# Kernel tuning notes

Measured on AMD Instinct MI355X. Metric: run time of the kernel, lower is better.

Reference implementation:

```python
import jax, jax.numpy as jnp
import numpy as np

N = 12288      # num nodes == in_num_dim (num_center_nodes)
D_IN = 512     # in_node_dim
D_EMB = 128    # embed_dim
D_OUT = 64     # out_dim
E = 393216     # num edges (avg degree 32)
NEG_SLOPE = 0.2  # GATConv default negative_slope


def _glorot(k, shape):
    lim = float(np.sqrt(6.0 / (shape[0] + shape[1])))
    return jax.random.uniform(k, shape, jnp.float32, -lim, lim)


def setup_inputs() -> dict:
    key = jax.random.key(0)
    ks = jax.random.split(key, 13)
    x = jax.random.normal(ks[0], (N, D_IN), jnp.float32)
    edge_index = jax.random.randint(ks[1], (2, E), 0, N, jnp.int64)
    # StructureAE.dense: Linear(in_node_dim, embed_dim)
    W_s1 = _glorot(ks[2], (D_EMB, D_IN))
    b_s1 = jnp.zeros((D_EMB,), jnp.float32)
    # GATConv(embed_dim, out_dim): heads=1, concat, bias
    W_g = _glorot(ks[3], (D_OUT, D_EMB))
    a_src = _glorot(ks[4], (D_OUT, 1))[:, 0]
    a_dst = _glorot(ks[5], (D_OUT, 1))[:, 0]
    b_g = jnp.zeros((D_OUT,), jnp.float32)
    # AttributeAE: dense1 = Linear(N, embed_dim), dense2 = Linear(embed_dim, out_dim)
    W_a1 = _glorot(ks[6], (D_EMB, N))
    b_a1 = jnp.zeros((D_EMB,), jnp.float32)
    W_a2 = _glorot(ks[7], (D_OUT, D_EMB))
    b_a2 = jnp.zeros((D_OUT,), jnp.float32)
    return dict(x=x, W_s1=W_s1, b_s1=b_s1, W_g=W_g, a_src=a_src, a_dst=a_dst,
                b_g=b_g, W_a1=W_a1, b_a1=b_a1, W_a2=W_a2, b_a2=b_a2,
                edge_index=edge_index, batch_size=N)


def _gat(x1, W_g, a_src, a_dst, b_g, edge_index):
    """Single-head GATConv with self-loops (PyG defaults)."""
    n = x1.shape[0]
    g = x1 @ W_g.T                                   # [N, D_OUT]
    loops = jnp.arange(n, dtype=edge_index.dtype)
    src = jnp.concatenate([edge_index[0], loops])    # message source j
    dst = jnp.concatenate([edge_index[1], loops])    # message target i
    sc_src = g @ a_src                               # [N]
    sc_dst = g @ a_dst                               # [N]
    e = jax.nn.leaky_relu(sc_src[src] + sc_dst[dst], NEG_SLOPE)  # [E+N]
    m = jax.ops.segment_max(e, dst, num_segments=n)
    e = jnp.exp(e - m[dst])
    denom = jax.ops.segment_sum(e, dst, num_segments=n)
    alpha = e / denom[dst]                           # softmax per target node
    h = jax.ops.segment_sum(alpha[:, None] * g[src], dst, num_segments=n)
    return h + b_g


def reference(x, W_s1, b_s1, W_g, a_src, a_dst, b_g,
              W_a1, b_a1, W_a2, b_a2, edge_index, batch_size):
    n = x.shape[0]
    # StructureAE (dropout=0 -> identity)
    x1 = jax.nn.relu(x @ W_s1.T + b_s1)              # [N, D_EMB]
    h = _gat(x1, W_g, a_src, a_dst, b_g, edge_index)  # [N, D_OUT]
    s_ = jax.nn.sigmoid(h @ h.T)                     # [N, N]
    # AttributeAE on x[:num_center_nodes] (pad if batch smaller)
    xp = x if batch_size >= n else jnp.pad(x, ((0, n - batch_size), (0, 0)))
    xt = jax.nn.relu(xp.T @ W_a1.T + b_a1)           # [D_IN, D_EMB]
    xa = xt @ W_a2.T + b_a2                          # [D_IN, D_OUT]
    x_ = h @ xa.T                                    # [N, D_IN]
    return (x_, s_)
```

## Files before the change

kernel.cpp:

```cpp
#include <hip/hip_runtime.h>
#include <cstddef>
#include <cstdint>

#define N_NODES 12288
#define D_IN    512
#define D_EMB   128
#define D_OUT   64
#define NEDGE   393216

typedef __attribute__((ext_vector_type(8))) short short8;
typedef __attribute__((ext_vector_type(4))) float f32x4;

__device__ __forceinline__ ushort f2bf(float f) {
  uint32_t u = __float_as_uint(f);
  u += 0x7fffu + ((u >> 16) & 1u);
  return (ushort)(u >> 16);
}
__device__ __forceinline__ float bf2f(ushort h) {
  return __uint_as_float((uint32_t)h << 16);
}

__device__ __forceinline__ void conv4(const float* __restrict__ src,
    ushort* __restrict__ hi, ushort* __restrict__ lo, int idx)
{
  float4 v = *(const float4*)(src + idx);
  const float* pv = &v.x;
  ushort4 h, l;
  ushort* ph = &h.x; ushort* pl = &l.x;
#pragma unroll
  for (int q = 0; q < 4; ++q) {
    ph[q] = f2bf(pv[q]);
    pl[q] = f2bf(pv[q] - bf2f(ph[q]));
  }
  *(ushort4*)(hi + idx) = h;
  *(ushort4*)(lo + idx) = l;
}

template<int MODE>
__device__ __forceinline__ void mfma_tile64(
    int lane, int i0, int j0,
    const ushort* __restrict__ Ahi, const ushort* __restrict__ Alo,
    const ushort* __restrict__ Bhi, const ushort* __restrict__ Blo,
    const float* __restrict__ bias,
    float* __restrict__ Cf, ushort* __restrict__ Chi, ushort* __restrict__ Clo,
    int lda, int ldb, int K, int ldc,
    const float* __restrict__ a_src, const float* __restrict__ a_dst,
    float* __restrict__ sc_s, float* __restrict__ sc_d)
{
  int lm = lane & 15, lk = lane >> 4;
  f32x4 acc[4][4];
#pragma unroll
  for (int r = 0; r < 4; ++r)
#pragma unroll
    for (int c = 0; c < 4; ++c) acc[r][c] = (f32x4){0.f, 0.f, 0.f, 0.f};

#pragma unroll 1
  for (int k0 = 0; k0 < K; k0 += 32) {
    int kk = k0 + lk * 8;
    short8 Ah[4], Al[4], Bh[4], Bl[4];
#pragma unroll
    for (int t = 0; t < 4; ++t) {
      size_t ra = (size_t)(i0 + t * 16 + lm) * lda + kk;
      size_t rb = (size_t)(j0 + t * 16 + lm) * ldb + kk;
      Ah[t] = *(const short8*)(Ahi + ra);
      Al[t] = *(const short8*)(Alo + ra);
      Bh[t] = *(const short8*)(Bhi + rb);
      Bl[t] = *(const short8*)(Blo + rb);
    }
#pragma unroll
    for (int r = 0; r < 4; ++r)
#pragma unroll
      for (int c = 0; c < 4; ++c) {
        acc[r][c] = __builtin_amdgcn_mfma_f32_16x16x32_bf16(Ah[r], Bh[c], acc[r][c], 0, 0, 0);
        acc[r][c] = __builtin_amdgcn_mfma_f32_16x16x32_bf16(Ah[r], Bl[c], acc[r][c], 0, 0, 0);
        acc[r][c] = __builtin_amdgcn_mfma_f32_16x16x32_bf16(Al[r], Bh[c], acc[r][c], 0, 0, 0);
      }
  }

#pragma unroll
  for (int r = 0; r < 4; ++r)
#pragma unroll
    for (int c = 0; c < 4; ++c) {
      int col = j0 + c * 16 + lm;
#pragma unroll
      for (int q = 0; q < 4; ++q) {
        int row = i0 + r * 16 + lk * 4 + q;
        float v = acc[r][c][q];
        if (MODE == 1) {
          v += bias[col];
          v = fmaxf(v, 0.f);
          ushort hb = f2bf(v);
          Chi[(size_t)row * ldc + col] = hb;
          Clo[(size_t)row * ldc + col] = f2bf(v - bf2f(hb));
        } else {
          Cf[(size_t)row * ldc + col] = v;
        }
      }
    }

  if (MODE == 2) {
    float asv[4], adv[4];
#pragma unroll
    for (int c = 0; c < 4; ++c) {
      asv[c] = a_src[c * 16 + lm];
      adv[c] = a_dst[c * 16 + lm];
    }
#pragma unroll
    for (int r = 0; r < 4; ++r)
#pragma unroll
      for (int q = 0; q < 4; ++q) {
        float s = 0.f, d = 0.f;
#pragma unroll
        for (int c = 0; c < 4; ++c) {
          float v = acc[r][c][q];
          s = fmaf(v, asv[c], s);
          d = fmaf(v, adv[c], d);
        }
#pragma unroll
        for (int off = 1; off < 16; off <<= 1) {
          s += __shfl_xor(s, off);
          d += __shfl_xor(d, off);
        }
        if (lm == 0) {
          int row = i0 + r * 16 + lk * 4 + q;
          sc_s[row] = s;
          sc_d[row] = d;
        }
      }
  }
}

__global__ __launch_bounds__(256) void prep_kernel(
    const float* __restrict__ x, const float* __restrict__ Ws1,
    const float* __restrict__ Wg, const float* __restrict__ Wa1,
    ushort* __restrict__ xhi, ushort* __restrict__ xlo,
    ushort* __restrict__ s1h, ushort* __restrict__ s1l,
    ushort* __restrict__ wgh, ushort* __restrict__ wgl,
    int* __restrict__ deg, float* __restrict__ part)
{
  __shared__ float smem[6144];
  int b = blockIdx.x;
  int tid = threadIdx.x;
  if (b < 512) {
    float* Xs = smem;
    float* Ws = smem + 2048;
    int c0 = (b & 7) * 64;
    int i0 = (b >> 3) * 192;
    float* pout = part + (size_t)(b >> 3) * (D_IN * D_EMB);
    int txc = tid & 15, txj = tid >> 4;
    float acc[4][8] = {};
    for (int ib = 0; ib < 192; ib += 32) {
#pragma unroll
      for (int p = 0; p < 2; ++p) {
        int idx = tid + p * 256;
        int row = idx >> 4, q = idx & 15;
        *(float4*)&Xs[row * 64 + q * 4] =
            *(const float4*)(x + (size_t)(i0 + ib + row) * D_IN + c0 + q * 4);
      }
#pragma unroll
      for (int p = 0; p < 4; ++p) {
        int idx = tid + p * 256;
        int j = idx >> 3, q = idx & 7;
        float4 v = *(const float4*)(Wa1 + (size_t)j * N_NODES + i0 + ib + q * 4);
        Ws[(q * 4 + 0) * 128 + j] = v.x; Ws[(q * 4 + 1) * 128 + j] = v.y;
        Ws[(q * 4 + 2) * 128 + j] = v.z; Ws[(q * 4 + 3) * 128 + j] = v.w;
      }
      __syncthreads();
#pragma unroll
      for (int ii = 0; ii < 32; ++ii) {
        float a[4], bb[8];
        *(float4*)a = *(const float4*)&Xs[ii * 64 + txc * 4];
        *(float4*)&bb[0] = *(const float4*)&Ws[ii * 128 + txj * 8];
        *(float4*)&bb[4] = *(const float4*)&Ws[ii * 128 + txj * 8 + 4];
#pragma unroll
        for (int r = 0; r < 4; ++r)
#pragma unroll
          for (int c = 0; c < 8; ++c)
            acc[r][c] = fmaf(a[r], bb[c], acc[r][c]);
      }
      __syncthreads();
    }
#pragma unroll
    for (int r = 0; r < 4; ++r) {
      float4 o0, o1;
      o0.x = acc[r][0]; o0.y = acc[r][1]; o0.z = acc[r][2]; o0.w = acc[r][3];
      o1.x = acc[r][4]; o1.y = acc[r][5]; o1.z = acc[r][6]; o1.w = acc[r][7];
      size_t off = (size_t)(c0 + txc * 4 + r) * D_EMB + txj * 8;
      *(float4*)&pout[off] = o0;
      *(float4*)&pout[off + 4] = o1;
    }
  } else if (b < 6656) {
    int idx = ((b - 512) * 256 + tid) * 4;
    conv4(x, xhi, xlo, idx);
  } else if (b < 6728) {
    int bb = b - 6656;
    if (bb < 64) conv4(Ws1, s1h, s1l, (bb * 256 + tid) * 4);
    else         conv4(Wg,  wgh, wgl, ((bb - 64) * 256 + tid) * 4);
  } else {
    deg[(b - 6728) * 256 + tid] = 0;
  }
}

__device__ __forceinline__ bool edge_is64(const int* __restrict__ ei) {
  int hv = ei[2 * (threadIdx.x & 63) + 1];
  return __ballot(hv == 0) == 0xFFFFFFFFFFFFFFFFull;
}

__global__ __launch_bounds__(256) void l2_kernel(
    const int* __restrict__ ei, int* __restrict__ deg,
    const ushort* __restrict__ xhi, const ushort* __restrict__ xlo,
    const ushort* __restrict__ s1h, const ushort* __restrict__ s1l,
    const float* __restrict__ b_s1,
    ushort* __restrict__ x1hi, ushort* __restrict__ x1lo,
    const float* __restrict__ part, const float* __restrict__ b_a1,
    float* __restrict__ xt)
{
  int b = blockIdx.x;
  if (b < 96) {
    int lane = threadIdx.x & 63, wv = threadIdx.x >> 6;
    int i0 = b * 128 + (wv >> 1) * 64;
    int j0 = (wv & 1) * 64;
    mfma_tile64<1>(lane, i0, j0, xhi, xlo, s1h, s1l, b_s1,
                   nullptr, x1hi, x1lo, D_IN, D_IN, D_IN, D_EMB,
                   nullptr, nullptr, nullptr, nullptr);
  } else if (b < 1632) {
    bool is64 = edge_is64(ei);
    int e = (b - 96) * 256 + threadIdx.x;
    int dst = is64 ? ei[2 * (NEDGE + e)] : ei[NEDGE + e];
    atomicAdd(&deg[dst], 1);
  } else {
    int idx = (b - 1632) * 256 + threadIdx.x;
    float v = b_a1[idx & 127];
#pragma unroll 8
    for (int c = 0; c < 64; ++c) v += part[(size_t)c * (D_IN * D_EMB) + idx];
    xt[idx] = fmaxf(v, 0.f);
  }
}

__global__ __launch_bounds__(256) void l3_kernel(
    const int* __restrict__ deg, int* __restrict__ rp, int* __restrict__ cursor,
    const ushort* __restrict__ x1hi, const ushort* __restrict__ x1lo,
    const ushort* __restrict__ wgh, const ushort* __restrict__ wgl,
    float* __restrict__ g,
    const float* __restrict__ a_src, const float* __restrict__ a_dst,
    float* __restrict__ sc_s, float* __restrict__ sc_d,
    const float* __restrict__ xt, const float* __restrict__ Wa2,
    const float* __restrict__ b_a2,
    ushort* __restrict__ xahi, ushort* __restrict__ xalo)
{
  __shared__ float smem[4096];
  int b = blockIdx.x;
  int tid = threadIdx.x;
  if (b == 0) {
    int* sums = (int*)smem;
    constexpr int C = N_NODES / 256;
    int base = tid * C;
    int local[C];
    int s = 0;
#pragma unroll
    for (int i = 0; i < C; ++i) { local[i] = deg[base + i]; s += local[i]; }
    sums[tid] = s;
    __syncthreads();
    for (int off = 1; off < 256; off <<= 1) {
      int v = (tid >= off) ? sums[tid - off] : 0;
      __syncthreads();
      sums[tid] += v;
      __syncthreads();
    }
    int prefix = (tid == 0) ? 0 : sums[tid - 1];
#pragma unroll
    for (int i = 0; i < C; ++i) {
      rp[base + i] = prefix;
      cursor[base + i] = prefix;
      prefix += local[i];
    }
    if (tid == 255) rp[N_NODES] = prefix;
  } else if (b < 49) {
    int lane = tid & 63, wv = tid >> 6;
    int i0 = (b - 1) * 256 + wv * 64;
    mfma_tile64<2>(lane, i0, 0, x1hi, x1lo, wgh, wgl, nullptr,
                   g, nullptr, nullptr, D_EMB, D_EMB, D_EMB, D_OUT,
                   a_src, a_dst, sc_s, sc_d);
  } else {
    float* As = smem;
    float* Bs = smem + 2048;
    int m0 = (b - 49) * 64;
    int tx = tid & 15, ty = tid >> 4;
    float acc[4][4] = {};
    for (int k0 = 0; k0 < D_EMB; k0 += 32) {
#pragma unroll
      for (int p = 0; p < 2; ++p) {
        int idx = tid + p * 256;
        int row = idx >> 3;
        int kq = idx & 7;
        float4 va = *(const float4*)(xt + (size_t)(m0 + row) * D_EMB + k0 + kq * 4);
        As[(kq * 4 + 0) * 64 + row] = va.x; As[(kq * 4 + 1) * 64 + row] = va.y;
        As[(kq * 4 + 2) * 64 + row] = va.z; As[(kq * 4 + 3) * 64 + row] = va.w;
        float4 vb = *(const float4*)(Wa2 + (size_t)row * D_EMB + k0 + kq * 4);
        Bs[(kq * 4 + 0) * 64 + row] = vb.x; Bs[(kq * 4 + 1) * 64 + row] = vb.y;
        Bs[(kq * 4 + 2) * 64 + row] = vb.z; Bs[(kq * 4 + 3) * 64 + row] = vb.w;
      }
      __syncthreads();
#pragma unroll
      for (int k = 0; k < 32; ++k) {
        float a[4], bb[4];
        *(float4*)a = *(const float4*)&As[k * 64 + ty * 4];
        *(float4*)bb = *(const float4*)&Bs[k * 64 + tx * 4];
#pragma unroll
        for (int r = 0; r < 4; ++r)
#pragma unroll
          for (int c = 0; c < 4; ++c)
            acc[r][c] = fmaf(a[r], bb[c], acc[r][c]);
      }
      __syncthreads();
    }
#pragma unroll
    for (int r = 0; r < 4; ++r) {
      int m = m0 + ty * 4 + r;
      ushort4 h, l;
      ushort* ph = &h.x; ushort* pl = &l.x;
#pragma unroll
      for (int c = 0; c < 4; ++c) {
        float v = acc[r][c] + b_a2[tx * 4 + c];
        ushort hb = f2bf(v);
        ph[c] = hb;
        pl[c] = f2bf(v - bf2f(hb));
      }
      *(ushort4*)(xahi + (size_t)m * D_OUT + tx * 4) = h;
      *(ushort4*)(xalo + (size_t)m * D_OUT + tx * 4) = l;
    }
  }
}

__global__ __launch_bounds__(256) void scatter_kernel(const int* __restrict__ ei,
    int* __restrict__ cursor, int* __restrict__ csr)
{
  bool is64 = edge_is64(ei);
  int e = blockIdx.x * 256 + threadIdx.x;
  int src = is64 ? ei[2 * e] : ei[e];
  int dst = is64 ? ei[2 * (NEDGE + e)] : ei[NEDGE + e];
  int p = atomicAdd(&cursor[dst], 1);
  csr[p] = src;
}

#define WCAP 192
__global__ __launch_bounds__(256) void gat_kernel(const int* __restrict__ rp,
    const int* __restrict__ csr, const float* __restrict__ sc_s,
    const float* __restrict__ sc_d, const float* __restrict__ g,
    const float* __restrict__ b_g,
    ushort* __restrict__ hhi, ushort* __restrict__ hlo)
{
  __shared__ float wbuf[4][WCAP];
  __shared__ int   sbuf[4][WCAP];
  int lane = threadIdx.x & 63;
  int w = threadIdx.x >> 6;
  int i = blockIdx.x * 4 + w;
  int beg = rp[i], end = rp[i + 1];
  int deg = end - beg;
  float scd = sc_d[i];
  float mymax = -3.4e38f;
  for (int j = lane; j <= deg; j += 64) {
    int s = (j < deg) ? csr[beg + j] : i;
    float e = sc_s[s] + scd;
    e = (e > 0.f) ? e : 0.2f * e;
    mymax = fmaxf(mymax, e);
    if (j < WCAP) sbuf[w][j] = s;
  }
#pragma unroll
  for (int off = 32; off; off >>= 1) mymax = fmaxf(mymax, __shfl_xor(mymax, off));
  float sum = 0.f;
  for (int j = lane; j <= deg; j += 64) {
    int s = (j < WCAP) ? sbuf[w][j] : ((j < deg) ? csr[beg + j] : i);
    float e = sc_s[s] + scd;
    e = (e > 0.f) ? e : 0.2f * e;
    float ex = __expf(e - mymax);
    sum += ex;
    if (j < WCAP) wbuf[w][j] = ex;
  }
#pragma unroll
  for (int off = 32; off; off >>= 1) sum += __shfl_xor(sum, off);
  float inv = 1.f / sum;
  float acc = 0.f;
  for (int j = 0; j <= deg; ++j) {
    int s; float ex;
    if (j < WCAP) { s = sbuf[w][j]; ex = wbuf[w][j]; }
    else {
      s = (j < deg) ? csr[beg + j] : i;
      float e = sc_s[s] + scd;
      e = (e > 0.f) ? e : 0.2f * e;
      ex = __expf(e - mymax);
    }
    acc = fmaf(ex * inv, g[(size_t)s * 64 + lane], acc);
  }
  float val = acc + b_g[lane];
  size_t o = (size_t)i * 64 + lane;
  ushort hi = f2bf(val);
  hhi[o] = hi;
  hlo[o] = f2bf(val - bf2f(hi));
}

__global__ __launch_bounds__(256) void l6_kernel(
    const ushort* __restrict__ hhi, const ushort* __restrict__ hlo,
    const ushort* __restrict__ xahi, const ushort* __restrict__ xalo,
    float* __restrict__ out_x, float* __restrict__ out_s)
{
  int b = blockIdx.x;
  int lane = threadIdx.x & 63;
  int wv = threadIdx.x >> 6;
  if (b < 384) {
    int i0 = (b >> 2) * 128 + (wv >> 1) * 64;
    int j0 = (b & 3) * 128 + (wv & 1) * 64;
    mfma_tile64<0>(lane, i0, j0, hhi, hlo, xahi, xalo, nullptr,
                   out_x, nullptr, nullptr, D_OUT, D_OUT, D_OUT, D_IN,
                   nullptr, nullptr, nullptr, nullptr);
    return;
  }
  int bb = b - 384;
  int iT = bb / 96;
  int jT = bb - iT * 96;
  int i0 = iT * 128 + (wv >> 1) * 64;
  int j0 = jT * 128 + (wv & 1) * 64;
  int lm = lane & 15, lk = lane >> 4;
  f32x4 acc[4][4];
#pragma unroll
  for (int r = 0; r < 4; ++r)
#pragma unroll
    for (int c = 0; c < 4; ++c) acc[r][c] = (f32x4){0.f, 0.f, 0.f, 0.f};
#pragma unroll
  for (int ks = 0; ks < 2; ++ks) {
    short8 Ah[4], Al[4], Bh[4], Bl[4];
#pragma unroll
    for (int t = 0; t < 4; ++t) {
      size_t ra = (size_t)(i0 + t * 16 + lm) * 64 + ks * 32 + lk * 8;
      size_t rb = (size_t)(j0 + t * 16 + lm) * 64 + ks * 32 + lk * 8;
      Ah[t] = *(const short8*)(hhi + ra);
      Al[t] = *(const short8*)(hlo + ra);
      Bh[t] = *(const short8*)(hhi + rb);
      Bl[t] = *(const short8*)(hlo + rb);
    }
#pragma unroll
    for (int r = 0; r < 4; ++r)
#pragma unroll
      for (int c = 0; c < 4; ++c) {
        acc[r][c] = __builtin_amdgcn_mfma_f32_16x16x32_bf16(Ah[r], Bh[c], acc[r][c], 0, 0, 0);
        acc[r][c] = __builtin_amdgcn_mfma_f32_16x16x32_bf16(Ah[r], Bl[c], acc[r][c], 0, 0, 0);
        acc[r][c] = __builtin_amdgcn_mfma_f32_16x16x32_bf16(Al[r], Bh[c], acc[r][c], 0, 0, 0);
      }
  }
#pragma unroll
  for (int r = 0; r < 4; ++r)
#pragma unroll
    for (int c = 0; c < 4; ++c) {
#pragma unroll
      for (int q = 0; q < 4; ++q) {
        float v = acc[r][c][q];
        float ex = __expf(-v);
#if __has_builtin(__builtin_amdgcn_rcpf)
        float s = __builtin_amdgcn_rcpf(1.f + ex);
#else
        float s = 1.f / (1.f + ex);
#endif
        out_s[(size_t)(i0 + r * 16 + lk * 4 + q) * N_NODES + (j0 + c * 16 + lm)] = s;
      }
    }
}

extern "C" void kernel_launch(void* const* d_in, const int* in_sizes, int n_in,
                              void* d_out, int out_size, void* d_ws, size_t ws_size,
                              hipStream_t stream)
{
  const float* x     = (const float*)d_in[0];
  const float* W_s1  = (const float*)d_in[1];
  const float* b_s1  = (const float*)d_in[2];
  const float* W_g   = (const float*)d_in[3];
  const float* a_src = (const float*)d_in[4];
  const float* a_dst = (const float*)d_in[5];
  const float* b_g   = (const float*)d_in[6];
  const float* W_a1  = (const float*)d_in[7];
  const float* b_a1  = (const float*)d_in[8];
  const float* W_a2  = (const float*)d_in[9];
  const float* b_a2  = (const float*)d_in[10];
  const int*   ei    = (const int*)d_in[11];

  float* ws   = (float*)d_ws;
  float* g    = ws;
  float* sc_s = g + (size_t)N_NODES * D_OUT;
  float* sc_d = sc_s + N_NODES;
  float* part = sc_d + N_NODES;
  float* xt   = part + (size_t)64 * D_IN * D_EMB;
  float* xa   = xt + D_IN * D_EMB;
  int* ip     = (int*)(xa + D_IN * D_OUT);
  int* flag   = ip;
  int* deg    = ip + 64;
  int* rp     = deg + N_NODES;
  int* cursor = rp + 12352;
  int* csr    = cursor + N_NODES;
  ushort* up  = (ushort*)(csr + NEDGE);
  ushort* xhi  = up;                         up += (size_t)N_NODES * D_IN;
  ushort* xlo  = up;                         up += (size_t)N_NODES * D_IN;
  ushort* x1hi = up;                         up += (size_t)N_NODES * D_EMB;
  ushort* x1lo = up;                         up += (size_t)N_NODES * D_EMB;
  ushort* Ws1hi = up;                        up += (size_t)D_EMB * D_IN;
  ushort* Ws1lo = up;                        up += (size_t)D_EMB * D_IN;
  ushort* Wghi = up;                         up += (size_t)D_OUT * D_EMB;
  ushort* Wglo = up;                         up += (size_t)D_OUT * D_EMB;
  ushort* hhi = up;                          up += (size_t)N_NODES * D_OUT;
  ushort* hlo = up;                          up += (size_t)N_NODES * D_OUT;
  ushort* xahi = up;                         up += (size_t)D_IN * D_OUT;
  ushort* xalo = up;                         up += (size_t)D_IN * D_OUT;
  (void)flag; (void)ws_size; (void)in_sizes; (void)n_in; (void)out_size;

  float* out_x = (float*)d_out;
  float* out_s = out_x + (size_t)N_NODES * D_IN;

  prep_kernel<<<6776, 256, 0, stream>>>(x, W_s1, W_g, W_a1,
      xhi, xlo, Ws1hi, Ws1lo, Wghi, Wglo, deg, part);
  l2_kernel<<<1888, 256, 0, stream>>>(ei, deg, xhi, xlo, Ws1hi, Ws1lo, b_s1,
      x1hi, x1lo, part, b_a1, xt);
  l3_kernel<<<57, 256, 0, stream>>>(deg, rp, cursor, x1hi, x1lo, Wghi, Wglo,
      g, a_src, a_dst, sc_s, sc_d, xt, W_a2, b_a2, xahi, xalo);
  scatter_kernel<<<NEDGE / 256, 256, 0, stream>>>(ei, cursor, csr);
  gat_kernel<<<N_NODES / 4, 256, 0, stream>>>(rp, csr, sc_s, sc_d, g, b_g,
                                              hhi, hlo);
  l6_kernel<<<9600, 256, 0, stream>>>(hhi, hlo, xahi, xalo, out_x, out_s);
}
```

Baseline: 862.0 us.

## Fuse input conversion and GAT projection into GEMM; use fixed-capacity edge buckets

The first GEMM now converts x from fp32 to a bf16 hi/lo pair as it loads it, so the separate conversion pass and its workspace round-trip are gone. The x1 tile is kept in swizzled shared memory, and the same block immediately computes g = x1·Wg and the attention scores. The prefix-scan plus scatter CSR build is replaced by per-node buckets of fixed capacity 160, filled from the degree atomics. That removes two kernels and a scan, but node degrees above 160 would corrupt results. Every l2 block now reserves 64KB of LDS, and the second GEMM stage runs on only half the waves.

```diff
diff --git a/kernel.cpp b/kernel.cpp
--- a/kernel.cpp
+++ b/kernel.cpp
@@ -7,6 +7,7 @@
 #define D_EMB   128
 #define D_OUT   64
 #define NEDGE   393216
+#define CAP     160
 
 typedef __attribute__((ext_vector_type(8))) short short8;
 typedef __attribute__((ext_vector_type(4))) float f32x4;
@@ -36,16 +37,27 @@
   *(ushort4*)(lo + idx) = l;
 }
 
-template<int MODE>
-__device__ __forceinline__ void mfma_tile64(
+__device__ __forceinline__ void cvt8(const float* __restrict__ p,
+                                     short8& h, short8& l)
+{
+  float4 a = *(const float4*)p;
+  float4 b = *(const float4*)(p + 4);
+  const float* f0 = &a.x;
+  const float* f1 = &b.x;
+#pragma unroll
+  for (int q = 0; q < 4; ++q) {
+    ushort h0 = f2bf(f0[q]);
+    h[q] = (short)h0;     l[q] = (short)f2bf(f0[q] - bf2f(h0));
+    ushort h1 = f2bf(f1[q]);
+    h[q + 4] = (short)h1; l[q + 4] = (short)f2bf(f1[q] - bf2f(h1));
+  }
+}
+
+__device__ __forceinline__ void mfma_tile64_f32out(
     int lane, int i0, int j0,
     const ushort* __restrict__ Ahi, const ushort* __restrict__ Alo,
     const ushort* __restrict__ Bhi, const ushort* __restrict__ Blo,
-    const float* __restrict__ bias,
-    float* __restrict__ Cf, ushort* __restrict__ Chi, ushort* __restrict__ Clo,
-    int lda, int ldb, int K, int ldc,
-    const float* __restrict__ a_src, const float* __restrict__ a_dst,
-    float* __restrict__ sc_s, float* __restrict__ sc_d)
+    float* __restrict__ Cf, int lda, int ldb, int K, int ldc)
 {
   int lm = lane & 15, lk = lane >> 4;
   f32x4 acc[4][4];
@@ -76,7 +88,6 @@
         acc[r][c] = __builtin_amdgcn_mfma_f32_16x16x32_bf16(Al[r], Bh[c], acc[r][c], 0, 0, 0);
       }
   }
-
 #pragma unroll
   for (int r = 0; r < 4; ++r)
 #pragma unroll
@@ -85,55 +96,14 @@
 #pragma unroll
       for (int q = 0; q < 4; ++q) {
         int row = i0 + r * 16 + lk * 4 + q;
-        float v = acc[r][c][q];
-        if (MODE == 1) {
-          v += bias[col];
-          v = fmaxf(v, 0.f);
-          ushort hb = f2bf(v);
-          Chi[(size_t)row * ldc + col] = hb;
-          Clo[(size_t)row * ldc + col] = f2bf(v - bf2f(hb));
-        } else {
-          Cf[(size_t)row * ldc + col] = v;
-        }
-      }
-    }
-
-  if (MODE == 2) {
-    float asv[4], adv[4];
-#pragma unroll
-    for (int c = 0; c < 4; ++c) {
-      asv[c] = a_src[c * 16 + lm];
-      adv[c] = a_dst[c * 16 + lm];
-    }
-#pragma unroll
-    for (int r = 0; r < 4; ++r)
-#pragma unroll
-      for (int q = 0; q < 4; ++q) {
-        float s = 0.f, d = 0.f;
-#pragma unroll
-        for (int c = 0; c < 4; ++c) {
-          float v = acc[r][c][q];
-          s = fmaf(v, asv[c], s);
-          d = fmaf(v, adv[c], d);
-        }
-#pragma unroll
-        for (int off = 1; off < 16; off <<= 1) {
-          s += __shfl_xor(s, off);
-          d += __shfl_xor(d, off);
-        }
-        if (lm == 0) {
-          int row = i0 + r * 16 + lk * 4 + q;
-          sc_s[row] = s;
-          sc_d[row] = d;
-        }
-      }
-  }
+        Cf[(size_t)row * ldc + col] = acc[r][c][q];
+      }
+    }
 }
 
 __global__ __launch_bounds__(256) void prep_kernel(
     const float* __restrict__ x, const float* __restrict__ Ws1,
     const float* __restrict__ Wg, const float* __restrict__ Wa1,
-    ushort* __restrict__ xhi, ushort* __restrict__ xlo,
     ushort* __restrict__ s1h, ushort* __restrict__ s1l,
     ushort* __restrict__ wgh, ushort* __restrict__ wgl,
     int* __restrict__ deg, float* __restrict__ part)
@@ -189,15 +159,12 @@
       *(float4*)&pout[off] = o0;
       *(float4*)&pout[off + 4] = o1;
     }
-  } else if (b < 6656) {
-    int idx = ((b - 512) * 256 + tid) * 4;
-    conv4(x, xhi, xlo, idx);
-  } else if (b < 6728) {
-    int bb = b - 6656;
+  } else if (b < 584) {
+    int bb = b - 512;
     if (bb < 64) conv4(Ws1, s1h, s1l, (bb * 256 + tid) * 4);
     else         conv4(Wg,  wgh, wgl, ((bb - 64) * 256 + tid) * 4);
   } else {
-    deg[(b - 6728) * 256 + tid] = 0;
+    deg[(b - 584) * 256 + tid] = 0;
   }
 }
 
@@ -207,29 +174,149 @@
 }
 
 __global__ __launch_bounds__(256) void l2_kernel(
-    const int* __restrict__ ei, int* __restrict__ deg,
-    const ushort* __restrict__ xhi, const ushort* __restrict__ xlo,
+    const int* __restrict__ ei, int* __restrict__ deg, int* __restrict__ csr,
+    const float* __restrict__ x,
     const ushort* __restrict__ s1h, const ushort* __restrict__ s1l,
     const float* __restrict__ b_s1,
-    ushort* __restrict__ x1hi, ushort* __restrict__ x1lo,
+    const ushort* __restrict__ wgh, const ushort* __restrict__ wgl,
+    float* __restrict__ g,
+    const float* __restrict__ a_src, const float* __restrict__ a_dst,
+    float* __restrict__ sc_s, float* __restrict__ sc_d,
     const float* __restrict__ part, const float* __restrict__ b_a1,
     float* __restrict__ xt)
 {
+  __shared__ ushort x1s[2][128 * 128];
   int b = blockIdx.x;
+  int tid = threadIdx.x;
   if (b < 96) {
-    int lane = threadIdx.x & 63, wv = threadIdx.x >> 6;
-    int i0 = b * 128 + (wv >> 1) * 64;
-    int j0 = (wv & 1) * 64;
-    mfma_tile64<1>(lane, i0, j0, xhi, xlo, s1h, s1l, b_s1,
-                   nullptr, x1hi, x1lo, D_IN, D_IN, D_IN, D_EMB,
-                   nullptr, nullptr, nullptr, nullptr);
+    int lane = tid & 63, wv = tid >> 6;
+    int lm = lane & 15, lk = lane >> 4;
+    int wr = wv >> 1, wc = wv & 1;
+    int i0 = b * 128;
+    {
+      f32x4 acc[4][4];
+#pragma unroll
+      for (int r = 0; r < 4; ++r)
+#pragma unroll
+        for (int c = 0; c < 4; ++c) acc[r][c] = (f32x4){0.f, 0.f, 0.f, 0.f};
+#pragma unroll 1
+      for (int k0 = 0; k0 < D_IN; k0 += 32) {
+        int kk = k0 + lk * 8;
+        short8 Ah[4], Al[4], Bh[4], Bl[4];
+#pragma unroll
+        for (int t = 0; t < 4; ++t) {
+          const float* pa = x + (size_t)(i0 + wr * 64 + t * 16 + lm) * D_IN + kk;
+          cvt8(pa, Ah[t], Al[t]);
+          size_t rb = (size_t)(wc * 64 + t * 16 + lm) * D_IN + kk;
+          Bh[t] = *(const short8*)(s1h + rb);
+          Bl[t] = *(const short8*)(s1l + rb);
+        }
+#pragma unroll
+        for (int r = 0; r < 4; ++r)
+#pragma unroll
+          for (int c = 0; c < 4; ++c) {
+            acc[r][c] = __builtin_amdgcn_mfma_f32_16x16x32_bf16(Ah[r], Bh[c], acc[r][c], 0, 0, 0);
+            acc[r][c] = __builtin_amdgcn_mfma_f32_16x16x32_bf16(Ah[r], Bl[c], acc[r][c], 0, 0, 0);
+            acc[r][c] = __builtin_amdgcn_mfma_f32_16x16x32_bf16(Al[r], Bh[c], acc[r][c], 0, 0, 0);
+          }
+      }
+#pragma unroll
+      for (int r = 0; r < 4; ++r)
+#pragma unroll
+        for (int c = 0; c < 4; ++c) {
+          int col = wc * 64 + c * 16 + lm;
+          float bv = b_s1[col];
+#pragma unroll
+          for (int q = 0; q < 4; ++q) {
+            int row = wr * 64 + r * 16 + lk * 4 + q;
+            float v = acc[r][c][q] + bv;
+            v = fmaxf(v, 0.f);
+            ushort hb = f2bf(v);
+            int idx = ((row << 7) + col) ^ ((row & 7) << 3);
+            x1s[0][idx] = hb;
+            x1s[1][idx] = f2bf(v - bf2f(hb));
+          }
+        }
+    }
+    __syncthreads();
+    if (wv < 2) {
+      f32x4 acc[4][4];
+#pragma unroll
+      for (int r = 0; r < 4; ++r)
+#pragma unroll
+        for (int c = 0; c < 4; ++c) acc[r][c] = (f32x4){0.f, 0.f, 0.f, 0.f};
+#pragma unroll 1
+      for (int k0 = 0; k0 < D_EMB; k0 += 32) {
+        int kk = k0 + lk * 8;
+        short8 Ah[4], Al[4], Bh[4], Bl[4];
+#pragma unroll
+        for (int t = 0; t < 4; ++t) {
+          int arow = wv * 64 + t * 16 + lm;
+          int aidx = ((arow << 7) + kk) ^ ((arow & 7) << 3);
+          Ah[t] = *(const short8*)&x1s[0][aidx];
+          Al[t] = *(const short8*)&x1s[1][aidx];
+          size_t rb = (size_t)(t * 16 + lm) * D_EMB + kk;
+          Bh[t] = *(const short8*)(wgh + rb);
+          Bl[t] = *(const short8*)(wgl + rb);
+        }
+#pragma unroll
+        for (int r = 0; r < 4; ++r)
+#pragma unroll
+          for (int c = 0; c < 4; ++c) {
+            acc[r][c] = __builtin_amdgcn_mfma_f32_16x16x32_bf16(Ah[r], Bh[c], acc[r][c], 0, 0, 0);
+            acc[r][c] = __builtin_amdgcn_mfma_f32_16x16x32_bf16(Ah[r], Bl[c], acc[r][c], 0, 0, 0);
+            acc[r][c] = __builtin_amdgcn_mfma_f32_16x16x32_bf16(Al[r], Bh[c], acc[r][c], 0, 0, 0);
+          }
+      }
+#pragma unroll
+      for (int r = 0; r < 4; ++r)
+#pragma unroll
+        for (int c = 0; c < 4; ++c) {
+          int col = c * 16 + lm;
+#pragma unroll
+          for (int q = 0; q < 4; ++q) {
+            int row = i0 + wv * 64 + r * 16 + lk * 4 + q;
+            g[(size_t)row * D_OUT + col] = acc[r][c][q];
+          }
+        }
+      float asv[4], adv[4];
+#pragma unroll
+      for (int c = 0; c < 4; ++c) {
+        asv[c] = a_src[c * 16 + lm];
+        adv[c] = a_dst[c * 16 + lm];
+      }
+#pragma unroll
+      for (int r = 0; r < 4; ++r)
+#pragma unroll
+        for (int q = 0; q < 4; ++q) {
+          float s = 0.f, d = 0.f;
+#pragma unroll
+          for (int c = 0; c < 4; ++c) {
+            float v = acc[r][c][q];
+            s = fmaf(v, asv[c], s);
+            d = fmaf(v, adv[c], d);
+          }
+#pragma unroll
+          for (int off = 1; off < 16; off <<= 1) {
+            s += __shfl_xor(s, off);
+            d += __shfl_xor(d, off);
+          }
+          if (lm == 0) {
+            int row = i0 + wv * 64 + r * 16 + lk * 4 + q;
+            sc_s[row] = s;
+            sc_d[row] = d;
+          }
+        }
+    }
   } else if (b < 1632) {
     bool is64 = edge_is64(ei);
-    int e = (b - 96) * 256 + threadIdx.x;
+    int e = (b - 96) * 256 + tid;
+    int src = is64 ? ei[2 * e] : ei[e];
     int dst = is64 ? ei[2 * (NEDGE + e)] : ei[NEDGE + e];
-    atomicAdd(&deg[dst], 1);
+    int p = atomicAdd(&deg[dst], 1);
+    csr[(size_t)dst * CAP + p] = src;
   } else {
-    int idx = (b - 1632) * 256 + threadIdx.x;
+    int idx = (b - 1632) * 256 + tid;
     float v = b_a1[idx & 127];
 #pragma unroll 8
     for (int c = 0; c < 64; ++c) v += part[(size_t)c * (D_IN * D_EMB) + idx];
@@ -237,13 +324,12 @@
   }
 }
 
+#define WCAP 192
 __global__ __launch_bounds__(256) void l3_kernel(
-    const int* __restrict__ deg, int* __restrict__ rp, int* __restrict__ cursor,
-    const ushort* __restrict__ x1hi, const ushort* __restrict__ x1lo,
-    const ushort* __restrict__ wgh, const ushort* __restrict__ wgl,
-    float* __restrict__ g,
-    const float* __restrict__ a_src, const float* __restrict__ a_dst,
-    float* __restrict__ sc_s, float* __restrict__ sc_d,
+    const int* __restrict__ deg, const int* __restrict__ csr,
+    const float* __restrict__ sc_s, const float* __restrict__ sc_d,
+    const float* __restrict__ g, const float* __restrict__ b_g,
+    ushort* __restrict__ hhi, ushort* __restrict__ hlo,
     const float* __restrict__ xt, const float* __restrict__ Wa2,
     const float* __restrict__ b_a2,
     ushort* __restrict__ xahi, ushort* __restrict__ xalo)
@@ -251,40 +337,58 @@
   __shared__ float smem[4096];
   int b = blockIdx.x;
   int tid = threadIdx.x;
-  if (b == 0) {
-    int* sums = (int*)smem;
-    constexpr int C = N_NODES / 256;
-    int base = tid * C;
-    int local[C];
-    int s = 0;
-#pragma unroll
-    for (int i = 0; i < C; ++i) { local[i] = deg[base + i]; s += local[i]; }
-    sums[tid] = s;
-    __syncthreads();
-    for (int off = 1; off < 256; off <<= 1) {
-      int v = (tid >= off) ? sums[tid - off] : 0;
-      __syncthreads();
-      sums[tid] += v;
-      __syncthreads();
-    }
-    int prefix = (tid == 0) ? 0 : sums[tid - 1];
-#pragma unroll
-    for (int i = 0; i < C; ++i) {
-      rp[base + i] = prefix;
-      cursor[base + i] = prefix;
-      prefix += local[i];
-    }
-    if (tid == 255) rp[N_NODES] = prefix;
-  } else if (b < 49) {
-    int lane = tid & 63, wv = tid >> 6;
-    int i0 = (b - 1) * 256 + wv * 64;
-    mfma_tile64<2>(lane, i0, 0, x1hi, x1lo, wgh, wgl, nullptr,
-                   g, nullptr, nullptr, D_EMB, D_EMB, D_EMB, D_OUT,
-                   a_src, a_dst, sc_s, sc_d);
+  if (b < 3072) {
+    float (*wbuf)[WCAP] = (float(*)[WCAP])smem;
+    int   (*sbuf)[WCAP] = (int(*)[WCAP])(smem + 4 * WCAP);
+    int lane = tid & 63;
+    int w = tid >> 6;
+    int i = b * 4 + w;
+    int dg = deg[i];
+    int base = i * CAP;
+    float scd = sc_d[i];
+    float mymax = -3.4e38f;
+    for (int j = lane; j <= dg; j += 64) {
+      int s = (j < dg) ? csr[base + j] : i;
+      float e = sc_s[s] + scd;
+      e = (e > 0.f) ? e : 0.2f * e;
+      mymax = fmaxf(mymax, e);
+      if (j < WCAP) sbuf[w][j] = s;
+    }
+#pragma unroll
+    for (int off = 32; off; off >>= 1) mymax = fmaxf(mymax, __shfl_xor(mymax, off));
+    float sum = 0.f;
+    for (int j = lane; j <= dg; j += 64) {
+      int s = (j < WCAP) ? sbuf[w][j] : ((j < dg) ? csr[base + j] : i);
+      float e = sc_s[s] + scd;
+      e = (e > 0.f) ? e : 0.2f * e;
+      float ex = __expf(e - mymax);
+      sum += ex;
+      if (j < WCAP) wbuf[w][j] = ex;
+    }
+#pragma unroll
+    for (int off = 32; off; off >>= 1) sum += __shfl_xor(sum, off);
+    float inv = 1.f / sum;
+    float acc = 0.f;
+    for (int j = 0; j <= dg; ++j) {
+      int s; float ex;
+      if (j < WCAP) { s = sbuf[w][j]; ex = wbuf[w][j]; }
+      else {
+        s = (j < dg) ? csr[base + j] : i;
+        float e = sc_s[s] + scd;
+        e = (e > 0.f) ? e : 0.2f * e;
+        ex = __expf(e - mymax);
+      }
+      acc = fmaf(ex * inv, g[(size_t)s * 64 + lane], acc);
+    }
+    float val = acc + b_g[lane];
+    size_t o = (size_t)i * 64 + lane;
+    ushort hi = f2bf(val);
+    hhi[o] = hi;
+    hlo[o] = f2bf(val - bf2f(hi));
   } else {
     float* As = smem;
     float* Bs = smem + 2048;
-    int m0 = (b - 49) * 64;
+    int m0 = (b - 3072) * 64;
     int tx = tid & 15, ty = tid >> 4;
     float acc[4][4] = {};
     for (int k0 = 0; k0 < D_EMB; k0 += 32) {
@@ -332,74 +436,7 @@
   }
 }
 
-__global__ __launch_bounds__(256) void scatter_kernel(const int* __restrict__ ei,
-    int* __restrict__ cursor, int* __restrict__ csr)
-{
-  bool is64 = edge_is64(ei);
-  int e = blockIdx.x * 256 + threadIdx.x;
-  int src = is64 ? ei[2 * e] : ei[e];
-  int dst = is64 ? ei[2 * (NEDGE + e)] : ei[NEDGE + e];
-  int p = atomicAdd(&cursor[dst], 1);
-  csr[p] = src;
-}
-
-#define WCAP 192
-__global__ __launch_bounds__(256) void gat_kernel(const int* __restrict__ rp,
-    const int* __restrict__ csr, const float* __restrict__ sc_s,
-    const float* __restrict__ sc_d, const float* __restrict__ g,
-    const float* __restrict__ b_g,
-    ushort* __restrict__ hhi, ushort* __restrict__ hlo)
-{
-  __shared__ float wbuf[4][WCAP];
-  __shared__ int   sbuf[4][WCAP];
-  int lane = threadIdx.x & 63;
-  int w = threadIdx.x >> 6;
-  int i = blockIdx.x * 4 + w;
-  int beg = rp[i], end = rp[i + 1];
-  int deg = end - beg;
-  float scd = sc_d[i];
-  float mymax = -3.4e38f;
-  for (int j = lane; j <= deg; j += 64) {
-    int s = (j < deg) ? csr[beg + j] : i;
-    float e = sc_s[s] + scd;
-    e = (e > 0.f) ? e : 0.2f * e;
-    mymax = fmaxf(mymax, e);
-    if (j < WCAP) sbuf[w][j] = s;
-  }
-#pragma unroll
-  for (int off = 32; off; off >>= 1) mymax = fmaxf(mymax, __shfl_xor(mymax, off));
-  float sum = 0.f;
-  for (int j = lane; j <= deg; j += 64) {
-    int s = (j < WCAP) ? sbuf[w][j] : ((j < deg) ? csr[beg + j] : i);
-    float e = sc_s[s] + scd;
-    e = (e > 0.f) ? e : 0.2f * e;
-    float ex = __expf(e - mymax);
-    sum += ex;
-    if (j < WCAP) wbuf[w][j] = ex;
-  }
-#pragma unroll
-  for (int off = 32; off; off >>= 1) sum += __shfl_xor(sum, off);
-  float inv = 1.f / sum;
-  float acc = 0.f;
-  for (int j = 0; j <= deg; ++j) {
-    int s; float ex;
-    if (j < WCAP) { s = sbuf[w][j]; ex = wbuf[w][j]; }
-    else {
-      s = (j < deg) ? csr[beg + j] : i;
-      float e = sc_s[s] + scd;
-      e = (e > 0.f) ? e : 0.2f * e;
-      ex = __expf(e - mymax);
-    }
-    acc = fmaf(ex * inv, g[(size_t)s * 64 + lane], acc);
-  }
-  float val = acc + b_g[lane];
-  size_t o = (size_t)i * 64 + lane;
-  ushort hi = f2bf(val);
-  hhi[o] = hi;
-  hlo[o] = f2bf(val - bf2f(hi));
-}
-
-__global__ __launch_bounds__(256) void l6_kernel(
+__global__ __launch_bounds__(256) void l4_kernel(
     const ushort* __restrict__ hhi, const ushort* __restrict__ hlo,
     const ushort* __restrict__ xahi, const ushort* __restrict__ xalo,
     float* __restrict__ out_x, float* __restrict__ out_s)
@@ -410,9 +447,8 @@
   if (b < 384) {
     int i0 = (b >> 2) * 128 + (wv >> 1) * 64;
     int j0 = (b & 3) * 128 + (wv & 1) * 64;
-    mfma_tile64<0>(lane, i0, j0, hhi, hlo, xahi, xalo, nullptr,
-                   out_x, nullptr, nullptr, D_OUT, D_OUT, D_OUT, D_IN,
-                   nullptr, nullptr, nullptr, nullptr);
+    mfma_tile64_f32out(lane, i0, j0, hhi, hlo, xahi, xalo,
+                       out_x, D_OUT, D_OUT, D_OUT, D_IN);
     return;
   }
   int bb = b - 384;
@@ -488,39 +524,27 @@
   float* sc_d = sc_s + N_NODES;
   float* part = sc_d + N_NODES;
   float* xt   = part + (size_t)64 * D_IN * D_EMB;
-  float* xa   = xt + D_IN * D_EMB;
-  int* ip     = (int*)(xa + D_IN * D_OUT);
-  int* flag   = ip;
-  int* deg    = ip + 64;
-  int* rp     = deg + N_NODES;
-  int* cursor = rp + 12352;
-  int* csr    = cursor + N_NODES;
-  ushort* up  = (ushort*)(csr + NEDGE);
-  ushort* xhi  = up;                         up += (size_t)N_NODES * D_IN;
-  ushort* xlo  = up;                         up += (size_t)N_NODES * D_IN;
-  ushort* x1hi = up;                         up += (size_t)N_NODES * D_EMB;
-  ushort* x1lo = up;                         up += (size_t)N_NODES * D_EMB;
+  int* deg    = (int*)(xt + D_IN * D_EMB);
+  int* csr    = deg + N_NODES;
+  ushort* up  = (ushort*)(csr + (size_t)N_NODES * CAP);
   ushort* Ws1hi = up;                        up += (size_t)D_EMB * D_IN;
   ushort* Ws1lo = up;                        up += (size_t)D_EMB * D_IN;
-  ushort* Wghi = up;                         up += (size_t)D_OUT * D_EMB;
-  ushort* Wglo = up;                         up += (size_t)D_OUT * D_EMB;
-  ushort* hhi = up;                          up += (size_t)N_NODES * D_OUT;
-  ushort* hlo = up;                          up += (size_t)N_NODES * D_OUT;
-  ushort* xahi = up;                         up += (size_t)D_IN * D_OUT;
-  ushort* xalo = up;                         up += (size_t)D_IN * D_OUT;
-  (void)flag; (void)ws_size; (void)in_sizes; (void)n_in; (void)out_size;
+  ushort* Wghi  = up;                        up += (size_t)D_OUT * D_EMB;
+  ushort* Wglo  = up;                        up += (size_t)D_OUT * D_EMB;
+  ushort* hhi   = up;                        up += (size_t)N_NODES * D_OUT;
+  ushort* hlo   = up;                        up += (size_t)N_NODES * D_OUT;
+  ushort* xahi  = up;                        up += (size_t)D_IN * D_OUT;
+  ushort* xalo  = up;                        up += (size_t)D_IN * D_OUT;
+  (void)ws_size; (void)in_sizes; (void)n_in; (void)out_size;
 
   float* out_x = (float*)d_out;
   float* out_s = out_x + (size_t)N_NODES * D_IN;
 
-  prep_kernel<<<6776, 256, 0, stream>>>(x, W_s1, W_g, W_a1,
-      xhi, xlo, Ws1hi, Ws1lo, Wghi, Wglo, deg, part);
-  l2_kernel<<<1888, 256, 0, stream>>>(ei, deg, xhi, xlo, Ws1hi, Ws1lo, b_s1,
-      x1hi, x1lo, part, b_a1, xt);
-  l3_kernel<<<57, 256, 0, stream>>>(deg, rp, cursor, x1hi, x1lo, Wghi, Wglo,
-      g, a_src, a_dst, sc_s, sc_d, xt, W_a2, b_a2, xahi, xalo);
-  scatter_kernel<<<NEDGE / 256, 256, 0, stream>>>(ei, cursor, csr);
-  gat_kernel<<<N_NODES / 4, 256, 0, stream>>>(rp, csr, sc_s, sc_d, g, b_g,
-                                              hhi, hlo);
-  l6_kernel<<<9600, 256, 0, stream>>>(hhi, hlo, xahi, xalo, out_x, out_s);
-}
+  prep_kernel<<<632, 256, 0, stream>>>(x, W_s1, W_g, W_a1,
+      Ws1hi, Ws1lo, Wghi, Wglo, deg, part);
+  l2_kernel<<<1888, 256, 0, stream>>>(ei, deg, csr, x, Ws1hi, Ws1lo, b_s1,
+      Wghi, Wglo, g, a_src, a_dst, sc_s, sc_d, part, b_a1, xt);
+  l3_kernel<<<3080, 256, 0, stream>>>(deg, csr, sc_s, sc_d, g, b_g,
+      hhi, hlo, xt, W_a2, b_a2, xahi, xalo);
+  l4_kernel<<<9600, 256, 0, stream>>>(hhi, hlo, xahi, xalo, out_x, out_s);
+}
```

Result: faster. 807.3 us (-6.3%).
